# Kernel tuning notes

Measured on AMD Instinct MI355X. Metric: run time of the kernel, lower is better.

## Reference

```python
import jax, jax.numpy as jnp
import numpy as np

B, S, D, H = 4, 1500, 1280, 20
HD = D // H  # 64

def setup_inputs() -> dict:
    key = jax.random.key(0)
    ks = jax.random.split(key, 8)
    scale = 1.0 / np.sqrt(D)
    return {
        "hidden_states": jax.random.normal(ks[0], (B, S, D), dtype=jnp.float32),
        "attention_mask": jnp.zeros((B, 1, S, S), dtype=jnp.float32),
        "q_w": jax.random.normal(ks[1], (D, D), dtype=jnp.float32) * scale,
        "q_b": jax.random.normal(ks[2], (D,), dtype=jnp.float32) * 0.02,
        "k_w": jax.random.normal(ks[3], (D, D), dtype=jnp.float32) * scale,
        "v_w": jax.random.normal(ks[4], (D, D), dtype=jnp.float32) * scale,
        "v_b": jax.random.normal(ks[5], (D,), dtype=jnp.float32) * 0.02,
        "o_w": jax.random.normal(ks[6], (D, D), dtype=jnp.float32) * scale,
        "o_b": jax.random.normal(ks[7], (D,), dtype=jnp.float32) * 0.02,
    }

def reference(hidden_states, attention_mask, q_w, q_b, k_w, v_w, v_b, o_w, o_b):
    bsz, seq_len, d_model = hidden_states.shape
    scaling = HD ** (-0.5)
    # Projections (k_proj has NO bias, matching the module)
    q = hidden_states @ q_w + q_b
    k = hidden_states @ k_w
    v = hidden_states @ v_w + v_b
    # [B, H, S, HD]
    q = q.reshape(bsz, seq_len, H, HD).transpose(0, 2, 1, 3)
    k = k.reshape(bsz, seq_len, H, HD).transpose(0, 2, 1, 3)
    v = v.reshape(bsz, seq_len, H, HD).transpose(0, 2, 1, 3)
    scores = jnp.einsum("bhqd,bhkd->bhqk", q, k) * scaling
    scores = scores + attention_mask
    attn = jax.nn.softmax(scores.astype(jnp.float32), axis=-1).astype(q.dtype)
    out = jnp.einsum("bhqk,bhkd->bhqd", attn, v)
    out = out.transpose(0, 2, 1, 3).reshape(bsz, seq_len, d_model)
    return out @ o_w + o_b
```

## Files before the change

### kernel.cpp

```cpp
#include <hip/hip_runtime.h>
#include <hip/hip_bf16.h>
#include <cstddef>

#define B_   4
#define S_   1500
#define D_   1280
#define H_   20
#define HD_  64
#define M_   (B_*S_)
#define SPAD 1536
#define BIGNEG (-1e30f)
#define LOG2E 1.44269504088896340736f
#define KVB  64
#define NTA  24

typedef short bf16x8 __attribute__((ext_vector_type(8)));
typedef float f32x4 __attribute__((ext_vector_type(4)));
typedef unsigned short u16;
typedef u16 u16x8 __attribute__((ext_vector_type(8)));
typedef unsigned int u32x4v __attribute__((ext_vector_type(4)));

#define MFMA __builtin_amdgcn_mfma_f32_16x16x32_bf16

__device__ __forceinline__ u16 f2bf(float f) {
  union { float f; unsigned u; } x; x.f = f;
  unsigned r = (x.u + 0x7fffu + ((x.u >> 16) & 1u)) >> 16;
  return (u16)r;
}

__device__ __forceinline__ unsigned cvtpk(float a, float b) {
  unsigned r;
  asm volatile("v_cvt_pk_bf16_f32 %0, %1, %2" : "=v"(r) : "v"(a), "v"(b));
  return r;
}

__device__ __forceinline__ void gl_lds16(const u16* g, u16* l) {
  typedef __attribute__((address_space(1))) const unsigned GU;
  typedef __attribute__((address_space(3))) unsigned LU;
  __builtin_amdgcn_global_load_lds((GU*)g, (LU*)l, 16, 0, 0);
}

__global__ __launch_bounds__(256) void k_conv(const float* __restrict__ X, u16* __restrict__ Y) {
  size_t i = (size_t)blockIdx.x * 256 + threadIdx.x;
  const float4* p = (const float4*)(X + i * 8);
  float4 a = p[0], b = p[1];
  u16x8 v;
  v[0]=f2bf(a.x); v[1]=f2bf(a.y); v[2]=f2bf(a.z); v[3]=f2bf(a.w);
  v[4]=f2bf(b.x); v[5]=f2bf(b.y); v[6]=f2bf(b.z); v[7]=f2bf(b.w);
  *(u16x8*)(Y + i * 8) = v;
}

__global__ __launch_bounds__(256) void k_trans4(const float* __restrict__ qw,
                                                const float* __restrict__ kw,
                                                const float* __restrict__ vw,
                                                const float* __restrict__ ow,
                                                u16* __restrict__ Wt) {
  const float* W = (blockIdx.z == 0) ? qw : (blockIdx.z == 1) ? kw
                   : (blockIdx.z == 2) ? vw : ow;
  u16* dst = Wt + (size_t)blockIdx.z * D_ * D_;
  __shared__ float t[32][33];
  int n0 = blockIdx.x * 32, k0 = blockIdx.y * 32;
  int tx = threadIdx.x & 31, ty = threadIdx.x >> 5;
  #pragma unroll
  for (int i = ty; i < 32; i += 8) t[i][tx] = W[(size_t)(k0 + i) * D_ + n0 + tx];
  __syncthreads();
  #pragma unroll
  for (int i = ty; i < 32; i += 8) dst[(size_t)(n0 + i) * D_ + k0 + tx] = f2bf(t[tx][i]);
}

__global__ __launch_bounds__(256) void k_vtrans(const u16* __restrict__ Vb, u16* __restrict__ Vt) {
  __shared__ u16 t[128][72];
  int bh = blockIdx.x, b = bh / H_, h = bh % H_;
  int s0 = blockIdx.y * 128;
  int tid = threadIdx.x;
  #pragma unroll
  for (int r = 0; r < 4; r++) {
    int sl = r * 32 + (tid >> 3);
    int s = s0 + sl; if (s > S_ - 1) s = S_ - 1;
    bf16x8 v = *(const bf16x8*)(Vb + ((size_t)(b * S_ + s)) * D_ + h * HD_ + (tid & 7) * 8);
    *(bf16x8*)&t[sl][(tid & 7) * 8] = v;
  }
  __syncthreads();
  #pragma unroll
  for (int r = 0; r < 4; r++) {
    int d = r * 16 + (tid >> 4);
    int ss = (tid & 15) * 8;
    u16x8 o;
    #pragma unroll
    for (int q = 0; q < 8; q++) {
      int sl = ss + q;
      int kk = ((sl >> 4) & 3) * 4 + (sl & 3) + ((sl >> 2) & 3) * 16 + (sl & 64);
      o[q] = t[kk][d];
    }
    *(u16x8*)(Vt + ((size_t)bh * HD_ + d) * SPAD + s0 + ss) = o;
  }
}

__global__ __launch_bounds__(256) void k_gemmqkv(const u16* __restrict__ A,
                                                 const u16* __restrict__ Wt,
                                                 const float* __restrict__ q_b,
                                                 const float* __restrict__ v_b,
                                                 u16* __restrict__ Qb) {
  __shared__ u16 As[2][128 * 64];
  __shared__ u16 Bs[2][128 * 64];
  int tid = threadIdx.x;
  int lane = tid & 63;
  int wv = tid >> 6;
  int l16 = lane & 15, lg = lane >> 4;
  int wr = wv >> 1, wc = wv & 1;
  int m0 = blockIdx.x * 128;
  int n0g = blockIdx.y * 128;
  int sel = blockIdx.y / 10;
  int nloc = n0g - sel * 1280;

  int srow = tid >> 3;
  int csw = ((tid & 7) ^ (srow & 7)) * 8;
  const u16* asrc = A + csw;
  const u16* bsrc = Wt + csw;
  int dbase = wv * 8 * 64;

  f32x4 acc[4][4] = {};

#define STAGEG(tt, bufb) do {                                            \
    int kk0 = (tt) * 64;                                                 \
    _Pragma("unroll")                                                    \
    for (int c = 0; c < 4; c++) {                                        \
      int row = srow + c * 32;                                           \
      int ar = m0 + row; if (ar > M_ - 1) ar = M_ - 1;                   \
      gl_lds16(asrc + (size_t)ar * D_ + kk0,                             \
               &As[bufb][0] + dbase + c * 2048);                         \
      gl_lds16(bsrc + (size_t)(n0g + row) * D_ + kk0,                    \
               &Bs[bufb][0] + dbase + c * 2048);                         \
    }                                                                    \
  } while (0)

  STAGEG(0, 0);
  __syncthreads();
  for (int t = 0; t < 20; t++) {
    int cb = t & 1;
    if (t < 19) STAGEG(t + 1, cb ^ 1);
    const u16* AsC = &As[cb][0];
    const u16* BsC = &Bs[cb][0];
    #pragma unroll
    for (int kk = 0; kk < 2; kk++) {
      int pcol = ((kk * 4 + lg) ^ (l16 & 7)) * 8;
      bf16x8 af[4], bf[4];
      #pragma unroll
      for (int m = 0; m < 4; m++)
        af[m] = *(const bf16x8*)&AsC[(wr * 64 + m * 16 + l16) * 64 + pcol];
      #pragma unroll
      for (int n = 0; n < 4; n++)
        bf[n] = *(const bf16x8*)&BsC[(wc * 64 + n * 16 + l16) * 64 + pcol];
      __builtin_amdgcn_s_setprio(1);
      #pragma unroll
      for (int m = 0; m < 4; m++)
        #pragma unroll
        for (int n = 0; n < 4; n++)
          acc[m][n] = MFMA(af[m], bf[n], acc[m][n], 0, 0, 0);
      __builtin_amdgcn_s_setprio(0);
    }
    __syncthreads();
  }
#undef STAGEG

  const float* bias = (sel == 0) ? q_b : v_b;
  float scl = (sel == 0) ? (0.125f * LOG2E) : 1.0f;
  u16* outb = Qb + (size_t)sel * ((size_t)M_ * D_);

  #pragma unroll
  for (int m = 0; m < 4; m++) {
    int row0 = m0 + wr * 64 + m * 16 + lg * 4;
    #pragma unroll
    for (int n = 0; n < 4; n++) {
      int colL = nloc + wc * 64 + n * 16 + l16;
      float bv = (sel == 1) ? 0.0f : bias[colL];
      #pragma unroll
      for (int j = 0; j < 4; j++) {
        int row = row0 + j;
        if (row < M_) {
          float v = (acc[m][n][j] + bv) * scl;
          outb[(size_t)row * D_ + colL] = f2bf(v);
        }
      }
    }
  }
}

__global__ __launch_bounds__(256) void k_gemmo(const u16* __restrict__ A,
                                               const u16* __restrict__ Wt,
                                               const float* __restrict__ bias,
                                               float* __restrict__ outp) {
  __shared__ u16 As[2][128 * 64];
  __shared__ u16 Bs[2][128 * 64];
  int tid = threadIdx.x;
  int lane = tid & 63;
  int wv = tid >> 6;
  int l16 = lane & 15, lg = lane >> 4;
  int wr = wv >> 1, wc = wv & 1;
  int m0 = blockIdx.x * 128, n0 = blockIdx.y * 128;

  int srow = tid >> 3;
  int csw = ((tid & 7) ^ (srow & 7)) * 8;
  const u16* asrc = A + csw;
  const u16* bsrc = Wt + csw;
  int dbase = wv * 8 * 64;

  f32x4 acc[4][4] = {};

#define STAGEG(tt, bufb) do {                                            \
    int kk0 = (tt) * 64;                                                 \
    _Pragma("unroll")                                                    \
    for (int c = 0; c < 4; c++) {                                        \
      int row = srow + c * 32;                                           \
      int ar = m0 + row; if (ar > M_ - 1) ar = M_ - 1;                   \
      gl_lds16(asrc + (size_t)ar * D_ + kk0,                             \
               &As[bufb][0] + dbase + c * 2048);                         \
      gl_lds16(bsrc + (size_t)(n0 + row) * D_ + kk0,                     \
               &Bs[bufb][0] + dbase + c * 2048);                         \
    }                                                                    \
  } while (0)

  STAGEG(0, 0);
  __syncthreads();
  for (int t = 0; t < 20; t++) {
    int cb = t & 1;
    if (t < 19) STAGEG(t + 1, cb ^ 1);
    const u16* AsC = &As[cb][0];
    const u16* BsC = &Bs[cb][0];
    #pragma unroll
    for (int kk = 0; kk < 2; kk++) {
      int pcol = ((kk * 4 + lg) ^ (l16 & 7)) * 8;
      bf16x8 af[4], bf[4];
      #pragma unroll
      for (int m = 0; m < 4; m++)
        af[m] = *(const bf16x8*)&AsC[(wr * 64 + m * 16 + l16) * 64 + pcol];
      #pragma unroll
      for (int n = 0; n < 4; n++)
        bf[n] = *(const bf16x8*)&BsC[(wc * 64 + n * 16 + l16) * 64 + pcol];
      __builtin_amdgcn_s_setprio(1);
      #pragma unroll
      for (int m = 0; m < 4; m++)
        #pragma unroll
        for (int n = 0; n < 4; n++)
          acc[m][n] = MFMA(af[m], bf[n], acc[m][n], 0, 0, 0);
      __builtin_amdgcn_s_setprio(0);
    }
    __syncthreads();
  }
#undef STAGEG

  #pragma unroll
  for (int m = 0; m < 4; m++) {
    int row0 = m0 + wr * 64 + m * 16 + lg * 4;
    #pragma unroll
    for (int n = 0; n < 4; n++) {
      int col = n0 + wc * 64 + n * 16 + l16;
      float bv = bias[col];
      #pragma unroll
      for (int j = 0; j < 4; j++) {
        int row = row0 + j;
        if (row < M_) outp[(size_t)row * D_ + col] = acc[m][n][j] + bv;
      }
    }
  }
}

__global__ __launch_bounds__(256) void k_attn(const u16* __restrict__ Qb,
                                              const u16* __restrict__ Kb,
                                              const u16* __restrict__ Vt,
                                              const float* __restrict__ mask,
                                              u16* __restrict__ Ctx) {
  __shared__ u16 Kl[2][64 * 64];
  __shared__ u16 Vl[2][64 * 64];

  int p = blockIdx.x;
  int L = (p & 7) * 120 + (p >> 3);
  int h = L % 20;
  int g = L / 20;
  int b = g / 12;
  int xq = g % 12;
  int bh = b * H_ + h;

  int tid = threadIdx.x;
  int lane = tid & 63, wv = tid >> 6;
  int l16 = lane & 15, lg = lane >> 4;
  int qw0 = xq * 128 + wv * 16;

  int qr0 = qw0 + l16;      if (qr0 > S_ - 1) qr0 = S_ - 1;
  int qr1 = qw0 + 64 + l16; if (qr1 > S_ - 1) qr1 = S_ - 1;
  const u16* qp0 = Qb + ((size_t)(b * S_ + qr0)) * D_ + h * HD_ + lg * 8;
  const u16* qp1 = Qb + ((size_t)(b * S_ + qr1)) * D_ + h * HD_ + lg * 8;
  bf16x8 aq00 = *(const bf16x8*)(qp0);
  bf16x8 aq01 = *(const bf16x8*)(qp0 + 32);
  bf16x8 aq10 = *(const bf16x8*)(qp1);
  bf16x8 aq11 = *(const bf16x8*)(qp1 + 32);
  const float* mrow0 = mask + (size_t)b * S_ * S_ + (size_t)qr0 * S_;
  const float* mrow1 = mask + (size_t)b * S_ * S_ + (size_t)qr1 * S_;

  int sr0 = wv * 16 + (lane >> 3);
  int csw = ((lane & 7) ^ (lane >> 3)) * 8;
  const u16* ksrc = Kb + (size_t)b * S_ * D_ + h * HD_ + csw;
  const u16* vsrc0 = Vt + ((size_t)bh * HD_ + sr0) * SPAD + csw;
  const u16* vsrc1 = vsrc0 + 8 * SPAD;

  float m0_ = BIGNEG, l0_ = 0.0f, m1_ = BIGNEG, l1_ = 0.0f;
  f32x4 acc0[4] = {}, acc1[4] = {};
  const f32x4 zf = {0, 0, 0, 0};
  float4 mvA[4], mvB[4];

#define STAGE(k0s, bufb) do {                                          \
    int key0_ = (k0s) + sr0;     if (key0_ > S_ - 1) key0_ = S_ - 1;   \
    int key1_ = key0_ + 8;       if (key1_ > S_ - 1) key1_ = S_ - 1;   \
    u16* kd_ = &Kl[bufb][0] + wv * 1024;                               \
    u16* vd_ = &Vl[bufb][0] + wv * 1024;                               \
    gl_lds16(ksrc + (size_t)key0_ * D_, kd_);                          \
    gl_lds16(ksrc + (size_t)key1_ * D_, kd_ + 512);                    \
    gl_lds16(vsrc0 + (k0s), vd_);                                      \
    gl_lds16(vsrc1 + (k0s), vd_ + 512);                                \
  } while (0)

#define SMX(sv, mm, ll, accv) do {                                     \
    float t0 = fmaxf(fmaxf(sv[0][0], sv[0][1]), fmaxf(sv[0][2], sv[0][3])); \
    float t1 = fmaxf(fmaxf(sv[1][0], sv[1][1]), fmaxf(sv[1][2], sv[1][3])); \
    float t2 = fmaxf(fmaxf(sv[2][0], sv[2][1]), fmaxf(sv[2][2], sv[2][3])); \
    float t3 = fmaxf(fmaxf(sv[3][0], sv[3][1]), fmaxf(sv[3][2], sv[3][3])); \
    float rmax = fmaxf(fmaxf(t0, t1), fmaxf(t2, t3));                  \
    rmax = fmaxf(rmax, __shfl_xor(rmax, 16));                          \
    rmax = fmaxf(rmax, __shfl_xor(rmax, 32));                          \
    float mn = fmaxf(mm, rmax);                                        \
    if (!__all(mn - mm <= 8.0f)) {                                     \
      float c = __builtin_amdgcn_exp2f(mm - mn);                       \
      mm = mn; ll *= c;                                                \
      _Pragma("unroll")                                                \
      for (int j = 0; j < 4; j++) {                                    \
        float cj = __shfl(c, lg * 4 + j);                              \
        accv[0][j] *= cj; accv[1][j] *= cj;                            \
        accv[2][j] *= cj; accv[3][j] *= cj;                            \
      }                                                                \
    }                                                                  \
    _Pragma("unroll")                                                  \
    for (int sub = 0; sub < 4; sub++)                                  \
      _Pragma("unroll")                                                \
      for (int j = 0; j < 4; j++)                                      \
        sv[sub][j] = __builtin_amdgcn_exp2f(sv[sub][j] - mm);          \
    float a0 = (sv[0][0] + sv[0][1]) + (sv[0][2] + sv[0][3]);          \
    float a1 = (sv[1][0] + sv[1][1]) + (sv[1][2] + sv[1][3]);          \
    float a2 = (sv[2][0] + sv[2][1]) + (sv[2][2] + sv[2][3]);          \
    float a3 = (sv[3][0] + sv[3][1]) + (sv[3][2] + sv[3][3]);          \
    float rs = (a0 + a1) + (a2 + a3);                                  \
    rs += __shfl_xor(rs, 16);                                          \
    rs += __shfl_xor(rs, 32);                                          \
    ll += rs;                                                          \
  } while (0)

#define COMPUTE(curb, k0_, LASTV) do {                                 \
    const u16* KlC = &Kl[curb][0];                                     \
    const u16* VlC = &Vl[curb][0];                                     \
    f32x4 s0[4], s1[4];                                                \
    __builtin_amdgcn_s_setprio(1);                                     \
    _Pragma("unroll")                                                  \
    for (int sub = 0; sub < 4; sub++) {                                \
      const u16* kb = KlC + (sub * 16 + l16) * 64;                     \
      bf16x8 kf0 = *(const bf16x8*)(kb + ((lg     ^ (l16 & 7)) * 8));  \
      bf16x8 kf1 = *(const bf16x8*)(kb + (((4+lg) ^ (l16 & 7)) * 8));  \
      s0[sub] = MFMA(kf0, aq00, zf, 0, 0, 0);                          \
      s0[sub] = MFMA(kf1, aq01, s0[sub], 0, 0, 0);                     \
      s1[sub] = MFMA(kf0, aq10, zf, 0, 0, 0);                          \
      s1[sub] = MFMA(kf1, aq11, s1[sub], 0, 0, 0);                     \
    }                                                                  \
    __builtin_amdgcn_s_setprio(0);                                     \
    _Pragma("unroll")                                                  \
    for (int sub = 0; sub < 4; sub++) {                                \
      s0[sub][0] = fmaf(mvA[sub].x, LOG2E, s0[sub][0]);                \
      s0[sub][1] = fmaf(mvA[sub].y, LOG2E, s0[sub][1]);                \
      s0[sub][2] = fmaf(mvA[sub].z, LOG2E, s0[sub][2]);                \
      s0[sub][3] = fmaf(mvA[sub].w, LOG2E, s0[sub][3]);                \
    }                                                                  \
    if (LASTV) {                                                       \
      _Pragma("unroll")                                                \
      for (int sub = 0; sub < 4; sub++) {                              \
        int kb_ = (k0_) + sub * 16 + lg * 4;                           \
        _Pragma("unroll")                                              \
        for (int j = 0; j < 4; j++)                                    \
          if (kb_ + j >= S_) s0[sub][j] = BIGNEG;                      \
      }                                                                \
    }                                                                  \
    SMX(s0, m0_, l0_, acc0);                                           \
    union { u32x4v u; bf16x8 bf; } pA0, pA1;                           \
    pA0.u[0] = cvtpk(s0[0][0], s0[0][1]); pA0.u[1] = cvtpk(s0[0][2], s0[0][3]); \
    pA0.u[2] = cvtpk(s0[1][0], s0[1][1]); pA0.u[3] = cvtpk(s0[1][2], s0[1][3]); \
    pA1.u[0] = cvtpk(s0[2][0], s0[2][1]); pA1.u[1] = cvtpk(s0[2][2], s0[2][3]); \
    pA1.u[2] = cvtpk(s0[3][0], s0[3][1]); pA1.u[3] = cvtpk(s0[3][2], s0[3][3]); \
    _Pragma("unroll")                                                  \
    for (int sub = 0; sub < 4; sub++) {                                \
      s1[sub][0] = fmaf(mvB[sub].x, LOG2E, s1[sub][0]);                \
      s1[sub][1] = fmaf(mvB[sub].y, LOG2E, s1[sub][1]);                \
      s1[sub][2] = fmaf(mvB[sub].z, LOG2E, s1[sub][2]);                \
      s1[sub][3] = fmaf(mvB[sub].w, LOG2E, s1[sub][3]);                \
    }                                                                  \
    if (LASTV) {                                                       \
      _Pragma("unroll")                                                \
      for (int sub = 0; sub < 4; sub++) {                              \
        int kb_ = (k0_) + sub * 16 + lg * 4;                           \
        _Pragma("unroll")                                              \
        for (int j = 0; j < 4; j++)                                    \
          if (kb_ + j >= S_) s1[sub][j] = BIGNEG;                      \
      }                                                                \
    }                                                                  \
    SMX(s1, m1_, l1_, acc1);                                           \
    union { u32x4v u; bf16x8 bf; } pB0, pB1;                           \
    pB0.u[0] = cvtpk(s1[0][0], s1[0][1]); pB0.u[1] = cvtpk(s1[0][2], s1[0][3]); \
    pB0.u[2] = cvtpk(s1[1][0], s1[1][1]); pB0.u[3] = cvtpk(s1[1][2], s1[1][3]); \
    pB1.u[0] = cvtpk(s1[2][0], s1[2][1]); pB1.u[1] = cvtpk(s1[2][2], s1[2][3]); \
    pB1.u[2] = cvtpk(s1[3][0], s1[3][1]); pB1.u[3] = cvtpk(s1[3][2], s1[3][3]); \
    __builtin_amdgcn_s_setprio(1);                                     \
    _Pragma("unroll")                                                  \
    for (int n = 0; n < 4; n++) {                                      \
      const u16* vb = VlC + (n * 16 + l16) * 64;                       \
      bf16x8 bv0 = *(const bf16x8*)(vb + (((lg*2  ) ^ (l16 & 7)) * 8));\
      bf16x8 bv1 = *(const bf16x8*)(vb + (((lg*2+1) ^ (l16 & 7)) * 8));\
      acc0[n] = MFMA(pA0.bf, bv0, acc0[n], 0, 0, 0);                   \
      acc0[n] = MFMA(pA1.bf, bv1, acc0[n], 0, 0, 0);                   \
      acc1[n] = MFMA(pB0.bf, bv0, acc1[n], 0, 0, 0);                   \
      acc1[n] = MFMA(pB1.bf, bv1, acc1[n], 0, 0, 0);                   \
    }                                                                  \
    __builtin_amdgcn_s_setprio(0);                                     \
  } while (0)

  STAGE(0, 0);
  #pragma unroll
  for (int sub = 0; sub < 4; sub++) {
    mvA[sub] = *(const float4*)(mrow0 + sub * 16 + lg * 4);
    mvB[sub] = *(const float4*)(mrow1 + sub * 16 + lg * 4);
  }
  asm volatile("" ::: "memory");

  for (int t = 0; t < NTA - 1; t++) {
    int k0 = t * KVB;
    int k1 = k0 + KVB;
    __builtin_amdgcn_s_barrier();
    asm volatile("" ::: "memory");
    STAGE(k1, (t + 1) & 1);
    float4 nA[4], nB[4];
    #pragma unroll
    for (int sub = 0; sub < 4; sub++) {
      int mc = k1 + sub * 16 + lg * 4; if (mc > S_ - 4) mc = S_ - 4;
      nA[sub] = *(const float4*)(mrow0 + mc);
      nB[sub] = *(const float4*)(mrow1 + mc);
    }
    asm volatile("s_waitcnt vmcnt(12)" ::: "memory");
    __builtin_amdgcn_s_barrier();
    asm volatile("" ::: "memory");
    COMPUTE(t & 1, k0, false);
    #pragma unroll
    for (int sub = 0; sub < 4; sub++) { mvA[sub] = nA[sub]; mvB[sub] = nB[sub]; }
  }
  {
    const int k0 = (NTA - 1) * KVB;
    __builtin_amdgcn_s_barrier();
    asm volatile("s_waitcnt vmcnt(8)" ::: "memory");
    __builtin_amdgcn_s_barrier();
    asm volatile("" ::: "memory");
    COMPUTE((NTA - 1) & 1, k0, true);
  }

  float inv0 = 1.0f / l0_;
  float inv1 = 1.0f / l1_;
  #pragma unroll
  for (int j = 0; j < 4; j++) {
    float ivj0 = __shfl(inv0, lg * 4 + j);
    float ivj1 = __shfl(inv1, lg * 4 + j);
    int row0 = qw0 + lg * 4 + j;
    int row1 = row0 + 64;
    if (row0 < S_) {
      #pragma unroll
      for (int n = 0; n < 4; n++)
        Ctx[((size_t)(b * S_ + row0)) * D_ + h * HD_ + n * 16 + l16] = f2bf(acc0[n][j] * ivj0);
    }
    if (row1 < S_) {
      #pragma unroll
      for (int n = 0; n < 4; n++)
        Ctx[((size_t)(b * S_ + row1)) * D_ + h * HD_ + n * 16 + l16] = f2bf(acc1[n][j] * ivj1);
    }
  }
#undef STAGE
#undef SMX
#undef COMPUTE
}

extern "C" void kernel_launch(void* const* d_in, const int* in_sizes, int n_in,
                              void* d_out, int out_size, void* d_ws, size_t ws_size,
                              hipStream_t stream) {
  const float* hs   = (const float*)d_in[0];
  const float* mask = (const float*)d_in[1];
  const float* q_w  = (const float*)d_in[2];
  const float* q_b  = (const float*)d_in[3];
  const float* k_w  = (const float*)d_in[4];
  const float* v_w  = (const float*)d_in[5];
  const float* v_b  = (const float*)d_in[6];
  const float* o_w  = (const float*)d_in[7];
  const float* o_b  = (const float*)d_in[8];
  float* out = (float*)d_out;

  char* w = (char*)d_ws;
  const size_t XD = (size_t)M_ * D_;
  const size_t WD = (size_t)D_ * D_;
  u16* Xb  = (u16*)(w);                 w += XD * 2;
  u16* Wtq = (u16*)(w);                 w += WD * 2;
  u16* Wtk = (u16*)(w);                 w += WD * 2;
  u16* Wtv = (u16*)(w);                 w += WD * 2;
  u16* Wto = (u16*)(w);                 w += WD * 2;
  u16* Qb  = (u16*)(w);                 w += XD * 2;
  u16* Kb  = (u16*)(w);                 w += XD * 2;
  u16* Vb  = (u16*)(w);                 w += XD * 2;
  u16* Vt  = (u16*)(w);                 w += (size_t)B_ * H_ * HD_ * SPAD * 2;
  u16* Ctx = Xb;
  (void)Wtk; (void)Wtv;

  k_conv<<<dim3(3750), dim3(256), 0, stream>>>(hs, Xb);
  k_trans4<<<dim3(40, 40, 4), dim3(256), 0, stream>>>(q_w, k_w, v_w, o_w, Wtq);

  k_gemmqkv<<<dim3(47, 30), dim3(256), 0, stream>>>(Xb, Wtq, q_b, v_b, Qb);
  k_vtrans<<<dim3(80, 12), dim3(256), 0, stream>>>(Vb, Vt);

  k_attn<<<dim3(960), dim3(256), 0, stream>>>(Qb, Kb, Vt, mask, Ctx);

  k_gemmo<<<dim3(47, 10), dim3(256), 0, stream>>>(Ctx, Wto, o_b, out);
}
```

Baseline: 276.1 us.

## Scan attention mask once and skip mask loads when a batch mask is all zero

Adds a pre-pass kernel that reads the whole attention mask once and sets a per-batch flag if any entry is nonzero. The attention kernel then skips the per-tile mask global loads and the mask FMAs for batches whose mask is all zero, and adjusts the vmcnt waits to match. This removes the mask traffic that every head currently re-reads. In exchange it adds a full mask read, a memset and an extra launch on every call. The masked path still runs when the mask contains nonzero values.

```diff
diff --git a/kernel.cpp b/kernel.cpp
--- a/kernel.cpp
+++ b/kernel.cpp
@@ -48,6 +48,19 @@
   v[0]=f2bf(a.x); v[1]=f2bf(a.y); v[2]=f2bf(a.z); v[3]=f2bf(a.w);
   v[4]=f2bf(b.x); v[5]=f2bf(b.y); v[6]=f2bf(b.z); v[7]=f2bf(b.w);
   *(u16x8*)(Y + i * 8) = v;
+}
+
+__global__ __launch_bounds__(256) void k_mscan(const float* __restrict__ m, int* __restrict__ flag) {
+  const size_t tot = (size_t)B_ * S_ * S_;
+  size_t i = ((size_t)blockIdx.x * 256 + threadIdx.x) * 4;
+  size_t stride = (size_t)gridDim.x * 256 * 4;
+  for (; i < tot; i += stride) {
+    float4 v = *(const float4*)(m + i);
+    if (v.x != 0.f || v.y != 0.f || v.z != 0.f || v.w != 0.f) {
+      int b = (int)(i / ((size_t)S_ * S_));
+      atomicOr(&flag[b], 1);
+    }
+  }
 }
 
 __global__ __launch_bounds__(256) void k_trans4(const float* __restrict__ qw,
@@ -269,6 +282,7 @@
                                               const u16* __restrict__ Kb,
                                               const u16* __restrict__ Vt,
                                               const float* __restrict__ mask,
+                                              const int* __restrict__ mflag,
                                               u16* __restrict__ Ctx) {
   __shared__ u16 Kl[2][64 * 64];
   __shared__ u16 Vl[2][64 * 64];
@@ -280,6 +294,7 @@
   int b = g / 12;
   int xq = g % 12;
   int bh = b * H_ + h;
+  int um = mflag[b];
 
   int tid = threadIdx.x;
   int lane = tid & 63, wv = tid >> 6;
@@ -307,6 +322,8 @@
   f32x4 acc0[4] = {}, acc1[4] = {};
   const f32x4 zf = {0, 0, 0, 0};
   float4 mvA[4], mvB[4];
+  #pragma unroll
+  for (int sub = 0; sub < 4; sub++) { mvA[sub] = make_float4(0,0,0,0); mvB[sub] = make_float4(0,0,0,0); }
 
 #define STAGE(k0s, bufb) do {                                          \
     int key0_ = (k0s) + sr0;     if (key0_ > S_ - 1) key0_ = S_ - 1;   \
@@ -369,12 +386,18 @@
       s1[sub] = MFMA(kf1, aq11, s1[sub], 0, 0, 0);                     \
     }                                                                  \
     __builtin_amdgcn_s_setprio(0);                                     \
-    _Pragma("unroll")                                                  \
-    for (int sub = 0; sub < 4; sub++) {                                \
-      s0[sub][0] = fmaf(mvA[sub].x, LOG2E, s0[sub][0]);                \
-      s0[sub][1] = fmaf(mvA[sub].y, LOG2E, s0[sub][1]);                \
-      s0[sub][2] = fmaf(mvA[sub].z, LOG2E, s0[sub][2]);                \
-      s0[sub][3] = fmaf(mvA[sub].w, LOG2E, s0[sub][3]);                \
+    if (um) {                                                          \
+      _Pragma("unroll")                                                \
+      for (int sub = 0; sub < 4; sub++) {                              \
+        s0[sub][0] = fmaf(mvA[sub].x, LOG2E, s0[sub][0]);              \
+        s0[sub][1] = fmaf(mvA[sub].y, LOG2E, s0[sub][1]);              \
+        s0[sub][2] = fmaf(mvA[sub].z, LOG2E, s0[sub][2]);              \
+        s0[sub][3] = fmaf(mvA[sub].w, LOG2E, s0[sub][3]);              \
+        s1[sub][0] = fmaf(mvB[sub].x, LOG2E, s1[sub][0]);              \
+        s1[sub][1] = fmaf(mvB[sub].y, LOG2E, s1[sub][1]);              \
+        s1[sub][2] = fmaf(mvB[sub].z, LOG2E, s1[sub][2]);              \
+        s1[sub][3] = fmaf(mvB[sub].w, LOG2E, s1[sub][3]);              \
+      }                                                                \
     }                                                                  \
     if (LASTV) {                                                       \
       _Pragma("unroll")                                                \
@@ -382,7 +405,7 @@
         int kb_ = (k0_) + sub * 16 + lg * 4;                           \
         _Pragma("unroll")                                              \
         for (int j = 0; j < 4; j++)                                    \
-          if (kb_ + j >= S_) s0[sub][j] = BIGNEG;                      \
+          if (kb_ + j >= S_) { s0[sub][j] = BIGNEG; s1[sub][j] = BIGNEG; } \
       }                                                                \
     }                                                                  \
     SMX(s0, m0_, l0_, acc0);                                           \
@@ -391,22 +414,6 @@
     pA0.u[2] = cvtpk(s0[1][0], s0[1][1]); pA0.u[3] = cvtpk(s0[1][2], s0[1][3]); \
     pA1.u[0] = cvtpk(s0[2][0], s0[2][1]); pA1.u[1] = cvtpk(s0[2][2], s0[2][3]); \
     pA1.u[2] = cvtpk(s0[3][0], s0[3][1]); pA1.u[3] = cvtpk(s0[3][2], s0[3][3]); \
-    _Pragma("unroll")                                                  \
-    for (int sub = 0; sub < 4; sub++) {                                \
-      s1[sub][0] = fmaf(mvB[sub].x, LOG2E, s1[sub][0]);                \
-      s1[sub][1] = fmaf(mvB[sub].y, LOG2E, s1[sub][1]);                \
-      s1[sub][2] = fmaf(mvB[sub].z, LOG2E, s1[sub][2]);                \
-      s1[sub][3] = fmaf(mvB[sub].w, LOG2E, s1[sub][3]);                \
-    }                                                                  \
-    if (LASTV) {                                                       \
-      _Pragma("unroll")                                                \
-      for (int sub = 0; sub < 4; sub++) {                              \
-        int kb_ = (k0_) + sub * 16 + lg * 4;                           \
-        _Pragma("unroll")                                              \
-        for (int j = 0; j < 4; j++)                                    \
-          if (kb_ + j >= S_) s1[sub][j] = BIGNEG;                      \
-      }                                                                \
-    }                                                                  \
     SMX(s1, m1_, l1_, acc1);                                           \
     union { u32x4v u; bf16x8 bf; } pB0, pB1;                           \
     pB0.u[0] = cvtpk(s1[0][0], s1[0][1]); pB0.u[1] = cvtpk(s1[0][2], s1[0][3]); \
@@ -428,10 +435,12 @@
   } while (0)
 
   STAGE(0, 0);
-  #pragma unroll
-  for (int sub = 0; sub < 4; sub++) {
-    mvA[sub] = *(const float4*)(mrow0 + sub * 16 + lg * 4);
-    mvB[sub] = *(const float4*)(mrow1 + sub * 16 + lg * 4);
+  if (um) {
+    #pragma unroll
+    for (int sub = 0; sub < 4; sub++) {
+      mvA[sub] = *(const float4*)(mrow0 + sub * 16 + lg * 4);
+      mvB[sub] = *(const float4*)(mrow1 + sub * 16 + lg * 4);
+    }
   }
   asm volatile("" ::: "memory");
 
@@ -442,23 +451,30 @@
     asm volatile("" ::: "memory");
     STAGE(k1, (t + 1) & 1);
     float4 nA[4], nB[4];
-    #pragma unroll
-    for (int sub = 0; sub < 4; sub++) {
-      int mc = k1 + sub * 16 + lg * 4; if (mc > S_ - 4) mc = S_ - 4;
-      nA[sub] = *(const float4*)(mrow0 + mc);
-      nB[sub] = *(const float4*)(mrow1 + mc);
-    }
-    asm volatile("s_waitcnt vmcnt(12)" ::: "memory");
+    if (um) {
+      #pragma unroll
+      for (int sub = 0; sub < 4; sub++) {
+        int mc = k1 + sub * 16 + lg * 4; if (mc > S_ - 4) mc = S_ - 4;
+        nA[sub] = *(const float4*)(mrow0 + mc);
+        nB[sub] = *(const float4*)(mrow1 + mc);
+      }
+      asm volatile("s_waitcnt vmcnt(12)" ::: "memory");
+    } else {
+      asm volatile("s_waitcnt vmcnt(4)" ::: "memory");
+    }
     __builtin_amdgcn_s_barrier();
     asm volatile("" ::: "memory");
     COMPUTE(t & 1, k0, false);
-    #pragma unroll
-    for (int sub = 0; sub < 4; sub++) { mvA[sub] = nA[sub]; mvB[sub] = nB[sub]; }
+    if (um) {
+      #pragma unroll
+      for (int sub = 0; sub < 4; sub++) { mvA[sub] = nA[sub]; mvB[sub] = nB[sub]; }
+    }
   }
   {
     const int k0 = (NTA - 1) * KVB;
     __builtin_amdgcn_s_barrier();
-    asm volatile("s_waitcnt vmcnt(8)" ::: "memory");
+    if (um) asm volatile("s_waitcnt vmcnt(8)" ::: "memory");
+    else    asm volatile("s_waitcnt vmcnt(0)" ::: "memory");
     __builtin_amdgcn_s_barrier();
     asm volatile("" ::: "memory");
     COMPUTE((NTA - 1) & 1, k0, true);
@@ -514,16 +530,20 @@
   u16* Kb  = (u16*)(w);                 w += XD * 2;
   u16* Vb  = (u16*)(w);                 w += XD * 2;
   u16* Vt  = (u16*)(w);                 w += (size_t)B_ * H_ * HD_ * SPAD * 2;
+  int* mflag = (int*)(w);               w += 4 * sizeof(int);
   u16* Ctx = Xb;
   (void)Wtk; (void)Wtv;
 
+  hipMemsetAsync(mflag, 0, 4 * sizeof(int), stream);
+  k_mscan<<<dim3(2048), dim3(256), 0, stream>>>(mask, mflag);
+
   k_conv<<<dim3(3750), dim3(256), 0, stream>>>(hs, Xb);
   k_trans4<<<dim3(40, 40, 4), dim3(256), 0, stream>>>(q_w, k_w, v_w, o_w, Wtq);
 
   k_gemmqkv<<<dim3(47, 30), dim3(256), 0, stream>>>(Xb, Wtq, q_b, v_b, Qb);
   k_vtrans<<<dim3(80, 12), dim3(256), 0, stream>>>(Vb, Vt);
 
-  k_attn<<<dim3(960), dim3(256), 0, stream>>>(Qb, Kb, Vt, mask, Ctx);
+  k_attn<<<dim3(960), dim3(256), 0, stream>>>(Qb, Kb, Vt, mask, mflag, Ctx);
 
   k_gemmo<<<dim3(47, 10), dim3(256), 0, stream>>>(Ctx, Wto, o_b, out);
 }
```

Result: faster. 266.7 us (-3.4%).
